# Performance work log

Measured on AMD Instinct MI355X. Metric: run time of the kernel, lower is better.

## Reference

```python
import jax, jax.numpy as jnp
import numpy as np

N_HEADS = 16
COORDS = 1024
K_DIM = COORDS // N_HEADS  # 64


def setup_inputs() -> dict:
    key = jax.random.key(0)
    k1, k2, k3, k4 = jax.random.split(key, 4)
    x = jax.random.normal(k1, (2, 2048, COORDS), dtype=jnp.float32)
    W_proj = jax.random.normal(k2, (COORDS, COORDS), dtype=jnp.float32) * 0.02
    pre_metric = jax.random.normal(k3, (N_HEADS, K_DIM, K_DIM), dtype=jnp.float32) + jnp.eye(K_DIM, dtype=jnp.float32) * 0.01
    W_mix = jax.random.normal(k4, (COORDS, COORDS), dtype=jnp.float32) * 0.02
    return {"in_sequence_bwc": x, "W_proj": W_proj, "pre_metric": pre_metric, "W_mix": W_mix}


def reference(in_sequence_bwc, W_proj, pre_metric, W_mix):
    b, w, c = in_sequence_bwc.shape
    n, k = N_HEADS, K_DIM
    neg_inf = jnp.float32(-jnp.inf)
    sqrt_k = jnp.sqrt(jnp.float32(k))

    # build per-head metric: lower-tri mask on pre_metric, row softmax, then P @ P^T
    tril_kk = jnp.tril(jnp.ones((k, k), dtype=bool))
    pm_nkk = jnp.where(tril_kk, pre_metric, neg_inf)
    pm_nkk = jax.nn.softmax(pm_nkk / sqrt_k, axis=-1)
    metric_nkk = pm_nkk @ jnp.swapaxes(pm_nkk, -1, -2)

    # shared projection used as Q, K and V (torch Linear: x @ W.T, no bias)
    proj_bwc = in_sequence_bwc @ W_proj.T
    proj_bnwk = proj_bwc.reshape(b, w, n, k).transpose(0, 2, 1, 3)  # [b,n,w,k]

    # bilinear scores: Q @ M @ K^T, scaled
    qm_bnwk = jnp.einsum('bnik,nkl->bnil', proj_bnwk, metric_nkk)
    scores_bnww = jnp.einsum('bnik,bnjk->bnij', qm_bnwk, proj_bnwk) / sqrt_k

    causal_ww = jnp.tril(jnp.ones((w, w), dtype=bool))
    scores_bnww = jnp.where(causal_ww[None, None], scores_bnww, neg_inf)
    att_bnww = jax.nn.softmax(scores_bnww, axis=-1)

    nudged_bnwk = att_bnww @ proj_bnwk
    nudged_bwc = nudged_bnwk.transpose(0, 2, 1, 3).reshape(b, w, c)
    return nudged_bwc @ W_mix.T
```

## Files before the change

kernel.cpp:

```cpp
#include <hip/hip_runtime.h>
#include <stdint.h>
#include <stddef.h>

typedef unsigned short u16;
typedef unsigned int u32;
typedef __attribute__((ext_vector_type(8))) __bf16 bf16x8;
typedef __attribute__((ext_vector_type(4))) float f32x4;
typedef __attribute__((ext_vector_type(16))) float f32x16;

#define DEV __device__ __forceinline__

#define BATCH 2
#define SEQ   2048
#define CDIM  1024
#define NH    16
#define KD    64
#define MROWS (BATCH * SEQ)
#define NX (MROWS * CDIM)
#define NW (CDIM * CDIM)
#define BHSZ  131072

DEV u16 f32_to_bf16(float f) {
  union { float f; unsigned u; } v; v.f = f;
  return (u16)((v.u + 0x7fffu + ((v.u >> 16) & 1u)) >> 16);
}
DEV u32 pack_bf16x2(float a, float b) {
  union { __bf16 h[2]; u32 u; } r;
  r.h[0] = (__bf16)a; r.h[1] = (__bf16)b;
  return r.u;
}
DEV u32 pack_trunc(float a, float b) {
  return __builtin_amdgcn_perm(__float_as_uint(b), __float_as_uint(a), 0x07060302u);
}
DEV float v_exp2(float x) {
  float r; asm("v_exp_f32 %0, %1" : "=v"(r) : "v"(x)); return r;
}

DEV void gl_lds16(const u16* g, u16* l) {
  __builtin_amdgcn_global_load_lds(
      (const __attribute__((address_space(1))) void*)(g),
      (__attribute__((address_space(3))) void*)(l), 16, 0, 0);
}


__global__ void cvt_metric(const float* __restrict__ x, const float* __restrict__ wp,
                           const float* __restrict__ wm, const float* __restrict__ pm,
                           u16* __restrict__ xb, u16* __restrict__ wpb,
                           u16* __restrict__ wmb, u16* __restrict__ metric) {
  __shared__ float P[64][65];
  int bid = blockIdx.x, t = threadIdx.x;
  if (bid < 2048) {
    int total4 = (NX + 2 * NW) >> 2;
    for (int i4 = bid * 256 + t; i4 < total4; i4 += 2048 * 256) {
      int i = i4 << 2;
      const float* src; u16* dst; int off;
      if (i < NX)           { src = x;  dst = xb;  off = i; }
      else if (i < NX + NW) { src = wp; dst = wpb; off = i - NX; }
      else                  { src = wm; dst = wmb; off = i - NX - NW; }
      float4 v = *reinterpret_cast<const float4*>(src + off);
      ushort4 o;
      o.x = f32_to_bf16(v.x); o.y = f32_to_bf16(v.y);
      o.z = f32_to_bf16(v.z); o.w = f32_to_bf16(v.w);
      *reinterpret_cast<ushort4*>(dst + off) = o;
    }
    return;
  }
  int mb = bid - 2048;
  int h = mb >> 4, jgrp = mb & 15;
  if (t < 64) {
    int i = t;
    const float* row = pm + (size_t)(h * 64 + i) * 64;
    float mx = -1e30f;
    for (int j = 0; j <= i; ++j) mx = fmaxf(mx, row[j] * 0.125f);
    float s = 0.f;
    for (int j = 0; j <= i; ++j) { float e = expf(row[j] * 0.125f - mx); P[i][j] = e; s += e; }
    float inv = 1.f / s;
    for (int j = 0; j <= i; ++j) P[i][j] *= inv;
    for (int j = i + 1; j < 64; ++j) P[i][j] = 0.f;
  }
  __syncthreads();
  {
    int i = t & 63, jq = t >> 6;
    int j = jgrp * 4 + jq;
    float acc = 0.f;
    #pragma unroll
    for (int l = 0; l < 64; ++l) acc += P[i][l] * P[j][l];
    metric[(size_t)h * 4096 + i * 64 + j] = f32_to_bf16(acc);
  }
}

template <int MODE>
__launch_bounds__(256)
__global__ void gemm_xwt(const u16* __restrict__ A, const u16* __restrict__ B,
                         void* __restrict__ C0, u16* __restrict__ C1,
                         const u16* __restrict__ Mbf, u16* __restrict__ Qf,
                         int M, int N, int K) {
  __shared__ __align__(16) u16 As[128 * 64];
  __shared__ __align__(16) u16 Bs[64 * 64];
  __shared__ __align__(16) u16 PlMl[MODE == 0 ? (128 * 72 + 64 * 72) : 16];
  u16* Pl = PlMl;
  u16* Ml = PlMl + 128 * 72;
  int bm0 = blockIdx.y * 128, bn0 = blockIdx.x * 64;
  int t = threadIdx.x, wv = t >> 6, lane = t & 63;
  int l15 = lane & 15, l4 = lane >> 4;
  f32x4 acc[2][4] = {};

  if (MODE == 0) {
    int h = bn0 >> 6;
    #pragma unroll
    for (int it = 0; it < 2; ++it) {
      int i = t * 8 + it * 2048;
      int r = i >> 6, c8 = i & 63;
      *reinterpret_cast<uint4*>(Ml + r * 72 + c8) =
          *reinterpret_cast<const uint4*>(Mbf + h * 4096 + i);
    }
  }

  const int r8 = lane >> 3;
  const int sseg = ((lane & 7) ^ r8) * 8;

  for (int k0 = 0; k0 < K; k0 += 64) {
    #pragma unroll
    for (int q = 0; q < 4; ++q) {
      int rowl = q * 32 + wv * 8;
      gl_lds16(A + (size_t)(bm0 + rowl + r8) * K + k0 + sseg, As + rowl * 64);
    }
    #pragma unroll
    for (int q = 0; q < 2; ++q) {
      int rowl = q * 32 + wv * 8;
      gl_lds16(B + (size_t)(bn0 + rowl + r8) * K + k0 + sseg, Bs + rowl * 64);
    }
    __syncthreads();
    #pragma unroll
    for (int kk = 0; kk < 2; ++kk) {
      bf16x8 af[2], bfm[4];
      #pragma unroll
      for (int m = 0; m < 2; ++m) {
        int R = wv * 32 + m * 16 + l15;
        af[m] = *reinterpret_cast<const bf16x8*>(As + R * 64 + ((kk * 4 + l4) ^ (R & 7)) * 8);
      }
      #pragma unroll
      for (int nn = 0; nn < 4; ++nn) {
        int R = nn * 16 + l15;
        bfm[nn] = *reinterpret_cast<const bf16x8*>(Bs + R * 64 + ((kk * 4 + l4) ^ (R & 7)) * 8);
      }
      #pragma unroll
      for (int m = 0; m < 2; ++m)
        #pragma unroll
        for (int nn = 0; nn < 4; ++nn)
          acc[m][nn] = __builtin_amdgcn_mfma_f32_16x16x32_bf16(af[m], bfm[nn], acc[m][nn], 0, 0, 0);
    }
    __syncthreads();
  }

  if (MODE == 0) {
    int h = bn0 >> 6, bb = bm0 >> 11;
    size_t base = (size_t)(bb * NH + h) * BHSZ;
    #pragma unroll
    for (int m = 0; m < 2; ++m) {
      #pragma unroll
      for (int nn = 0; nn < 4; ++nn) {
        #pragma unroll
        for (int rr = 0; rr < 4; ++rr) {
          int rowl = wv * 32 + m * 16 + l4 * 4 + rr;
          int d = nn * 16 + l15;
          u16 hv = f32_to_bf16(acc[m][nn][rr]);
          int w2 = (bm0 & 2047) + rowl;
          int tile = w2 >> 6, rt = w2 & 63;
          int rl = rt & 31;
          int rls = (rl & 19) | ((rl & 4) << 1) | ((rl & 8) >> 1);
          ((u16*)C0)[base + (size_t)(tile * 8 + (d >> 4) * 2 + (rt >> 5)) * 512
                     + (rls | (((d >> 3) & 1) << 5)) * 8 + (d & 7)] = hv;
          C1[base + (size_t)(tile * 8 + ((rt >> 4) & 3) * 2 + (d >> 5)) * 512
             + ((d & 31) | (((rt >> 3) & 1) << 5)) * 8 + (rt & 7)] = hv;
          Pl[rowl * 72 + d] = hv;
        }
      }
    }
    __syncthreads();
    const float cl2 = 0.125f * 1.44269504088896f;
    f32x4 acc2[2][4] = {};
    #pragma unroll
    for (int kk2 = 0; kk2 < 2; ++kk2) {
      bf16x8 af2[2], bm2[4];
      #pragma unroll
      for (int m = 0; m < 2; ++m)
        af2[m] = *reinterpret_cast<const bf16x8*>(Pl + (wv * 32 + m * 16 + l15) * 72 + kk2 * 32 + l4 * 8);
      #pragma unroll
      for (int nn = 0; nn < 4; ++nn)
        bm2[nn] = *reinterpret_cast<const bf16x8*>(Ml + (nn * 16 + l15) * 72 + kk2 * 32 + l4 * 8);
      #pragma unroll
      for (int m = 0; m < 2; ++m)
        #pragma unroll
        for (int nn = 0; nn < 4; ++nn)
          acc2[m][nn] = __builtin_amdgcn_mfma_f32_16x16x32_bf16(af2[m], bm2[nn], acc2[m][nn], 0, 0, 0);
    }
    #pragma unroll
    for (int m = 0; m < 2; ++m) {
      #pragma unroll
      for (int nn = 0; nn < 4; ++nn) {
        #pragma unroll
        for (int rr = 0; rr < 4; ++rr) {
          int rowl = wv * 32 + m * 16 + l4 * 4 + rr;
          int d = nn * 16 + l15;
          int w2 = (bm0 & 2047) + rowl;
          Qf[base + (size_t)((w2 >> 5) * 4 + (d >> 4)) * 512
             + ((w2 & 31) | (((d >> 3) & 1) << 5)) * 8 + (d & 7)]
              = f32_to_bf16(acc2[m][nn][rr] * cl2);
        }
      }
    }
  } else {
    #pragma unroll
    for (int m = 0; m < 2; ++m) {
      int rbase = bm0 + wv * 32 + m * 16 + l4 * 4;
      #pragma unroll
      for (int nn = 0; nn < 4; ++nn) {
        int col = bn0 + nn * 16 + l15;
        #pragma unroll
        for (int rr = 0; rr < 4; ++rr)
          ((float*)C0)[(size_t)(rbase + rr) * N + col] = acc[m][nn][rr];
      }
    }
  }
}

__launch_bounds__(256)
__global__ void attn_kernel(const u16* __restrict__ Qf, const u16* __restrict__ Kf,
                            const u16* __restrict__ Vf, u16* __restrict__ nudged) {
  const int bh = blockIdx.x;
  const int bb = bh >> 4, h = bh & 15;
  const int p = 63 - (int)blockIdx.y;
  const int t = threadIdx.x, wv = t >> 6, lane = t & 63;
  const int c = lane & 31, hi = lane >> 5;
  const int q0 = p * 32;

  __shared__ float smf[4][2176];

  const u16* __restrict__ Kbh = Kf + (size_t)bh * BHSZ;
  const u16* __restrict__ Vbh = Vf + (size_t)bh * BHSZ;

  bf16x8 qf[4];
  {
    const u16* __restrict__ Qb = Qf + (size_t)bh * BHSZ + p * 2048 + lane * 8;
    #pragma unroll
    for (int kc = 0; kc < 4; ++kc)
      qf[kc] = *reinterpret_cast<const bf16x8*>(Qb + kc * 512);
  }

  f32x16 o0 = {}, o1 = {};
  float sv0 = 0.f, sv1 = 0.f;

  const int half = wv & 1;
  u32 koff = (u32)((wv >> 1) * 4096 + half * 512 + lane * 8);
  u32 voff = (u32)((wv >> 1) * 4096 + half * 2048 + lane * 8);

  bf16x8 kf[4], vf0[2], vf1[2];
  if (wv <= p) {
    #pragma unroll
    for (int kc = 0; kc < 4; ++kc)
      kf[kc] = *reinterpret_cast<const bf16x8*>(Kbh + koff + kc * 1024);
    #pragma unroll
    for (int ksl = 0; ksl < 2; ++ksl) {
      vf0[ksl] = *reinterpret_cast<const bf16x8*>(Vbh + voff + ksl * 1024);
      vf1[ksl] = *reinterpret_cast<const bf16x8*>(Vbh + voff + ksl * 1024 + 512);
    }
  }

  for (int T = wv; T <= p; T += 4) {
    f32x16 s = {};
    __builtin_amdgcn_s_setprio(1);
    #pragma unroll
    for (int kc = 0; kc < 4; ++kc)
      s = __builtin_amdgcn_mfma_f32_32x32x16_bf16(kf[kc], qf[kc], s, 0, 0, 0);
    __builtin_amdgcn_s_setprio(0);
    if (T + 4 <= p) {
      #pragma unroll
      for (int kc = 0; kc < 4; ++kc)
        kf[kc] = *reinterpret_cast<const bf16x8*>(Kbh + koff + 8192 + kc * 1024);
    }
    if (T == p) {
      #pragma unroll
      for (int r = 0; r < 16; ++r) {
        int kvl = (r & 3) + 4 * ((r >> 2) & 1) + 8 * hi + 16 * (r >> 3);
        if (kvl > c) s[r] = -1e30f;
      }
    }
    u32 w[4][2];
    #pragma unroll
    for (int g = 0; g < 4; ++g) {
      float a = v_exp2(s[g * 4 + 0]);
      float b = v_exp2(s[g * 4 + 1]);
      float cc = v_exp2(s[g * 4 + 2]);
      float d = v_exp2(s[g * 4 + 3]);
      sv0 += a + b; sv1 += cc + d;
      w[g][0] = pack_trunc(a, b);
      w[g][1] = pack_trunc(cc, d);
    }
    bf16x8 pa[2];
    #pragma unroll
    for (int ksl = 0; ksl < 2; ++ksl) {
      union { u32 u[4]; bf16x8 v; } pk;
      pk.u[0] = w[2 * ksl][0];
      pk.u[1] = w[2 * ksl][1];
      pk.u[2] = w[2 * ksl + 1][0];
      pk.u[3] = w[2 * ksl + 1][1];
      pa[ksl] = pk.v;
    }
    __builtin_amdgcn_s_setprio(1);
    #pragma unroll
    for (int ksl = 0; ksl < 2; ++ksl) {
      o0 = __builtin_amdgcn_mfma_f32_32x32x16_bf16(vf0[ksl], pa[ksl], o0, 0, 0, 0);
      o1 = __builtin_amdgcn_mfma_f32_32x32x16_bf16(vf1[ksl], pa[ksl], o1, 0, 0, 0);
    }
    __builtin_amdgcn_s_setprio(0);
    if (T + 4 <= p) {
      #pragma unroll
      for (int ksl = 0; ksl < 2; ++ksl) {
        vf0[ksl] = *reinterpret_cast<const bf16x8*>(Vbh + voff + 8192 + ksl * 1024);
        vf1[ksl] = *reinterpret_cast<const bf16x8*>(Vbh + voff + 8192 + ksl * 1024 + 512);
      }
    }
    koff += 8192; voff += 8192;
  }

  float lrow;
  {
    float s2 = sv0 + sv1;
    lrow = s2 + __shfl_xor(s2, 32);
  }

  {
    float* Ob = smf[wv];
    #pragma unroll
    for (int r = 0; r < 16; ++r) {
      int d = (r & 3) + 8 * (r >> 2) + 4 * hi;
      Ob[d * 33 + c] = o0[r];
      Ob[(d + 32) * 33 + c] = o1[r];
    }
    if (hi == 0) Ob[2112 + c] = lrow;
  }
  __syncthreads();
  {
    int q = t >> 3, dseg = t & 7;
    float lsum = smf[0][2112 + q] + smf[1][2112 + q] + smf[2][2112 + q] + smf[3][2112 + q];
    float invd = 1.f / lsum;
    u16 outv[8];
    #pragma unroll
    for (int i2 = 0; i2 < 8; ++i2) {
      int d = dseg * 8 + i2;
      float v = smf[0][d * 33 + q] + smf[1][d * 33 + q] + smf[2][d * 33 + q] + smf[3][d * 33 + q];
      outv[i2] = f32_to_bf16(v * invd);
    }
    u16* dstp = nudged + ((size_t)bb * SEQ + q0 + q) * CDIM + h * KD + dseg * 8;
    uint4 ov;
    ov.x = (u32)outv[0] | ((u32)outv[1] << 16);
    ov.y = (u32)outv[2] | ((u32)outv[3] << 16);
    ov.z = (u32)outv[4] | ((u32)outv[5] << 16);
    ov.w = (u32)outv[6] | ((u32)outv[7] << 16);
    *reinterpret_cast<uint4*>(dstp) = ov;
  }
}

extern "C" void kernel_launch(void* const* d_in, const int* in_sizes, int n_in,
                              void* d_out, int out_size, void* d_ws, size_t ws_size,
                              hipStream_t stream) {
  (void)in_sizes; (void)n_in; (void)out_size; (void)ws_size;
  const float* x      = (const float*)d_in[0];
  const float* Wproj  = (const float*)d_in[1];
  const float* premet = (const float*)d_in[2];
  const float* Wmix   = (const float*)d_in[3];

  char* w = (char*)d_ws;
  u16* x_bf   = (u16*)w;  w += (size_t)MROWS * CDIM * 2;
  u16* wp_bf  = (u16*)w;  w += (size_t)CDIM * CDIM * 2;
  u16* wm_bf  = (u16*)w;  w += (size_t)CDIM * CDIM * 2;
  u16* metric = (u16*)w;  w += (size_t)NH * KD * KD * 2;
  u16* Kf     = (u16*)w;  w += (size_t)BATCH * NH * BHSZ * 2;
  u16* Vf     = (u16*)w;  w += (size_t)BATCH * NH * BHSZ * 2;
  u16* Qf     = (u16*)w;  w += (size_t)BATCH * NH * BHSZ * 2;
  u16* nudged = (u16*)w;  w += (size_t)MROWS * CDIM * 2;

  hipLaunchKernelGGL(cvt_metric, dim3(2304), dim3(256), 0, stream,
                     x, Wproj, Wmix, premet, x_bf, wp_bf, wm_bf, metric);
  hipLaunchKernelGGL((gemm_xwt<0>), dim3(CDIM / 64, MROWS / 128), dim3(256), 0, stream,
                     x_bf, wp_bf, (void*)Kf, Vf, metric, Qf, MROWS, CDIM, CDIM);
  hipLaunchKernelGGL(attn_kernel, dim3(32, 64), dim3(256), 0, stream,
                     Qf, Kf, Vf, nudged);
  hipLaunchKernelGGL((gemm_xwt<1>), dim3(CDIM / 64, MROWS / 128), dim3(256), 0, stream,
                     nudged, wm_bf, d_out, nullptr, nullptr, nullptr, MROWS, CDIM, CDIM);
}
```

Measured before the change: 97.60 us.

## Software-pipeline QK^T one tile ahead of softmax/PV in attention loop

```diff
diff --git a/kernel.cpp b/kernel.cpp
--- a/kernel.cpp
+++ b/kernel.cpp
@@ -252,34 +252,39 @@
   float sv0 = 0.f, sv1 = 0.f;
 
   const int half = wv & 1;
-  u32 koff = (u32)((wv >> 1) * 4096 + half * 512 + lane * 8);
-  u32 voff = (u32)((wv >> 1) * 4096 + half * 2048 + lane * 8);
+  const u32 kbase = (u32)((wv >> 1) * 4096 + half * 512 + lane * 8);
+  const u32 vbase = (u32)((wv >> 1) * 4096 + half * 2048 + lane * 8);
 
   bf16x8 kf[4], vf0[2], vf1[2];
-  if (wv <= p) {
+  f32x16 sA, sB;
+
+  const int cnt = (wv <= p) ? (((p - wv) >> 2) + 1) : 0;
+
+  auto ldK = [&](int j) {
+    u32 off = kbase + (u32)j * 8192;
     #pragma unroll
     for (int kc = 0; kc < 4; ++kc)
-      kf[kc] = *reinterpret_cast<const bf16x8*>(Kbh + koff + kc * 1024);
+      kf[kc] = *reinterpret_cast<const bf16x8*>(Kbh + off + kc * 1024);
+  };
+  auto ldV = [&](int j) {
+    u32 off = vbase + (u32)j * 8192;
     #pragma unroll
     for (int ksl = 0; ksl < 2; ++ksl) {
-      vf0[ksl] = *reinterpret_cast<const bf16x8*>(Vbh + voff + ksl * 1024);
-      vf1[ksl] = *reinterpret_cast<const bf16x8*>(Vbh + voff + ksl * 1024 + 512);
-    }
-  }
-
-  for (int T = wv; T <= p; T += 4) {
-    f32x16 s = {};
+      vf0[ksl] = *reinterpret_cast<const bf16x8*>(Vbh + off + ksl * 1024);
+      vf1[ksl] = *reinterpret_cast<const bf16x8*>(Vbh + off + ksl * 1024 + 512);
+    }
+  };
+  auto qk = [&](f32x16& s) {
+    f32x16 r = {};
     __builtin_amdgcn_s_setprio(1);
     #pragma unroll
     for (int kc = 0; kc < 4; ++kc)
-      s = __builtin_amdgcn_mfma_f32_32x32x16_bf16(kf[kc], qf[kc], s, 0, 0, 0);
+      r = __builtin_amdgcn_mfma_f32_32x32x16_bf16(kf[kc], qf[kc], r, 0, 0, 0);
     __builtin_amdgcn_s_setprio(0);
-    if (T + 4 <= p) {
-      #pragma unroll
-      for (int kc = 0; kc < 4; ++kc)
-        kf[kc] = *reinterpret_cast<const bf16x8*>(Kbh + koff + 8192 + kc * 1024);
-    }
-    if (T == p) {
+    s = r;
+  };
+  auto sm_pv = [&](f32x16& s, int Tg) {
+    if (Tg == p) {
       #pragma unroll
       for (int r = 0; r < 16; ++r) {
         int kvl = (r & 3) + 4 * ((r >> 2) & 1) + 8 * hi + 16 * (r >> 3);
@@ -314,15 +319,27 @@
       o1 = __builtin_amdgcn_mfma_f32_32x32x16_bf16(vf1[ksl], pa[ksl], o1, 0, 0, 0);
     }
     __builtin_amdgcn_s_setprio(0);
-    if (T + 4 <= p) {
-      #pragma unroll
-      for (int ksl = 0; ksl < 2; ++ksl) {
-        vf0[ksl] = *reinterpret_cast<const bf16x8*>(Vbh + voff + 8192 + ksl * 1024);
-        vf1[ksl] = *reinterpret_cast<const bf16x8*>(Vbh + voff + 8192 + ksl * 1024 + 512);
-      }
-    }
-    koff += 8192; voff += 8192;
-  }
+  };
+
+  if (cnt > 0) {
+    ldK(0); ldV(0);
+    qk(sA);
+    if (cnt > 1) ldK(1);
+  }
+  int ii = 0;
+  for (; ii + 2 <= cnt; ii += 2) {
+    qk(sB);
+    if (ii + 2 < cnt) ldK(ii + 2);
+    sm_pv(sA, wv + 4 * ii);
+    ldV(ii + 1);
+    if (ii + 2 < cnt) {
+      qk(sA);
+      if (ii + 3 < cnt) ldK(ii + 3);
+    }
+    sm_pv(sB, wv + 4 * (ii + 1));
+    if (ii + 2 < cnt) ldV(ii + 2);
+  }
+  if (ii < cnt) sm_pv(sA, wv + 4 * ii);
 
   float lrow;
   {
```

Measured after the change: 96.61 us. About the same (-1.0%).
